# Performance work log

Measured on AMD Instinct MI355X. Metric: run time of the kernel, lower is better.

The kernel has to match this reference:

```python
import jax, jax.numpy as jnp
import numpy as np
import math

L, B, T, S, D, H = 6, 4, 1024, 1024, 1024, 16
HD = D // H
SCALE = 1.0 / math.sqrt(HD)
EPS = 1e-5


def _ln(x, w, b):
    m = x.mean(-1, keepdims=True)
    v = ((x - m) ** 2).mean(-1, keepdims=True)
    return (x - m) * jax.lax.rsqrt(v + EPS) * w + b


def _mha(xq, xkv, qw, qb, kw, kb, vw, vb, ow, ob, mask):
    b, t, _ = xq.shape
    s = xkv.shape[1]
    q = (xq @ qw.T + qb).reshape(b, t, H, HD).transpose(0, 2, 1, 3)
    k = (xkv @ kw.T + kb).reshape(b, s, H, HD).transpose(0, 2, 1, 3)
    v = (xkv @ vw.T + vb).reshape(b, s, H, HD).transpose(0, 2, 1, 3)
    scores = jnp.einsum('bhqd,bhkd->bhqk', q, k) * SCALE
    scores = jnp.where(mask == 0, -jnp.inf, scores)
    attn = jax.nn.softmax(scores, axis=-1)  # dropout is identity (eval)
    o = jnp.einsum('bhqk,bhkd->bhqd', attn, v).transpose(0, 2, 1, 3).reshape(b, t, D)
    return o @ ow.T + ob


def _ffn(x, f1w, f1b, f2w, f2b, fnw, fnb):
    h = jax.nn.gelu(x @ f1w.T + f1b, approximate=False)
    y = h @ f2w.T + f2b
    return x + _ln(y, fnw, fnb)


def setup_inputs() -> dict:
    key = jax.random.key(0)
    ks = jax.random.split(key, 16)
    wf = lambda k: jax.random.normal(k, (L, D, D), jnp.float32) * 0.02
    zb = jnp.zeros((L, D), jnp.float32)
    ones = jnp.ones((L, D), jnp.float32)
    inp = {
        'x': jax.random.normal(ks[0], (B, T, D), jnp.float32),
        'enc_outputs': jax.random.normal(ks[1], (B, S, D), jnp.float32),
        'sqw': wf(ks[2]), 'sqb': zb, 'skw': wf(ks[3]), 'skb': zb,
        'svw': wf(ks[4]), 'svb': zb, 'sow': wf(ks[5]), 'sob': zb,
        'cqw': wf(ks[6]), 'cqb': zb, 'ckw': wf(ks[7]), 'ckb': zb,
        'cvw': wf(ks[8]), 'cvb': zb, 'cow': wf(ks[9]), 'cob': zb,
        'f1w': wf(ks[10]), 'f1b': zb, 'f2w': wf(ks[11]), 'f2b': zb,
        'fnw': ones, 'fnb': zb,
        'l1w': ones, 'l1b': zb, 'l2w': ones, 'l2b': zb, 'l3w': ones, 'l3b': zb,
        'src_mask': jnp.ones((1, 1, T, S), jnp.int32),
        'tgt_mask': jnp.tril(jnp.ones((T, T), jnp.int32))[None, None],
    }
    return inp


def reference(x, enc_outputs, sqw, sqb, skw, skb, svw, svb, sow, sob,
              cqw, cqb, ckw, ckb, cvw, cvb, cow, cob,
              f1w, f1b, f2w, f2b, fnw, fnb,
              l1w, l1b, l2w, l2b, l3w, l3b, src_mask, tgt_mask):
    for l in range(L):
        sa = _mha(x, x, sqw[l], sqb[l], skw[l], skb[l], svw[l], svb[l], sow[l], sob[l], tgt_mask)
        x = _ln(x + sa, l1w[l], l1b[l])
        ca = _mha(x, enc_outputs, cqw[l], cqb[l], ckw[l], ckb[l], cvw[l], cvb[l], cow[l], cob[l], src_mask)
        x = _ln(x + ca, l2w[l], l2b[l])
        ff = _ffn(x, f1w[l], f1b[l], f2w[l], f2b[l], fnw[l], fnb[l])
        x = _ln(x + ff, l3w[l], l3b[l])
    return x
```

## Files before the change

kernel.cpp:

```cpp
#include <hip/hip_runtime.h>
#include <stdint.h>

typedef unsigned short u16;
typedef unsigned int u32;
typedef __bf16 bf16x8 __attribute__((ext_vector_type(8)));
typedef float f32x4 __attribute__((ext_vector_type(4)));
typedef u16 u16x8 __attribute__((ext_vector_type(8)));
typedef u16 u16x4 __attribute__((ext_vector_type(4)));
typedef u32 u32x2 __attribute__((ext_vector_type(2)));

#define MFMA16(A, B, C) __builtin_amdgcn_mfma_f32_16x16x32_bf16((A), (B), (C), 0, 0, 0)

#define GLOAD_LDS16(GP, LP)                                                    \
  __builtin_amdgcn_global_load_lds(                                            \
      (__attribute__((address_space(1))) void*)(GP),                           \
      (__attribute__((address_space(3))) void*)(LP), 16, 0, 0)

__device__ __forceinline__ u16 f2bf(float f) {
  return __builtin_bit_cast(u16, (__bf16)f);
}

__device__ __forceinline__ float bf2f(u16 v) {
  return __builtin_bit_cast(float, ((u32)v) << 16);
}

__device__ __forceinline__ float exp2_raw(float x) {
  float r;
  asm("v_exp_f32 %0, %1\n\ts_nop 0" : "=v"(r) : "v"(x));
  return r;
}

__device__ __forceinline__ u32 cvt_pk_bf16(float lo, float hi) {
  u32 r;
  asm("v_cvt_pk_bf16_f32 %0, %1, %2" : "=v"(r) : "v"(lo), "v"(hi));
  return r;
}

#define SC2 0.1803368801111204f

struct WPtrs {
  const float* p[10];
};

__global__ __launch_bounds__(256) void wcvt_kernel(WPtrs w, u16* __restrict__ dst, int loff,
                                                   int nIter, int perMatUnits) {
  const int mat = blockIdx.y;
  const float4* __restrict__ src = (const float4*)(w.p[mat] + loff);
  u16x8* __restrict__ d = (u16x8*)dst + (size_t)mat * perMatUnits;
  size_t t = (size_t)blockIdx.x * 256 + threadIdx.x;
  for (int it = 0; it < nIter; ++it, t += 65536) {
    float4 v0 = src[t * 2];
    float4 v1 = src[t * 2 + 1];
    u16x8 o = {f2bf(v0.x), f2bf(v0.y), f2bf(v0.z), f2bf(v0.w),
               f2bf(v1.x), f2bf(v1.y), f2bf(v1.z), f2bf(v1.w)};
    d[t] = o;
  }
}

struct GemmArgs {
  const u16* A[3];
  const u16* W[3];
  const float* bias[3];
  u16* C[3];
  float scale[3];
};

__global__ __launch_bounds__(256, 4) void gemm_bt(GemmArgs g) {
  const int mat = blockIdx.y >> 3;
  const int n0 = (blockIdx.y & 7) * 128;
  const int m0 = blockIdx.x * 128;
  const int kz = blockIdx.z;
  const int kn = 16 / gridDim.z;
  const u16* __restrict__ A = g.A[mat];
  const u16* __restrict__ W = g.W[mat];

  __shared__ u16 As[128][64];
  __shared__ u16 Bs[128][64];

  const int tid = threadIdx.x;
  const int lane = tid & 63;
  const int wv = tid >> 6;
  const int wm = (wv >> 1) * 64;
  const int wn = (wv & 1) * 64;
  const int fr = lane & 15;
  const int fg = lane >> 4;

  f32x4 acc[4][4];
#pragma unroll
  for (int i = 0; i < 4; ++i)
#pragma unroll
    for (int j = 0; j < 4; ++j)
#pragma unroll
      for (int r = 0; r < 4; ++r) acc[i][j][r] = 0.f;

  const int row8 = lane >> 3;
  const int csw = ((lane & 7) ^ row8) * 8;
  const u16* ga = A + (size_t)(m0 + wv * 32 + row8) * 1024 + csw + kz * kn * 64;
  const u16* gb = W + (size_t)(n0 + wv * 32 + row8) * 1024 + csw + kz * kn * 64;

  for (int kt = 0; kt < kn; ++kt) {
    __syncthreads();
#pragma unroll
    for (int i = 0; i < 4; ++i) {
      GLOAD_LDS16(ga + (size_t)i * 8 * 1024, &As[wv * 32 + i * 8][0]);
      GLOAD_LDS16(gb + (size_t)i * 8 * 1024, &Bs[wv * 32 + i * 8][0]);
    }
    ga += 64;
    gb += 64;
    __syncthreads();
#pragma unroll
    for (int ks = 0; ks < 2; ++ks) {
      bf16x8 af[4], bfr[4];
#pragma unroll
      for (int i = 0; i < 4; ++i) {
        af[i] = *(const bf16x8*)&As[wm + i * 16 + fr][((ks * 4 + fg) ^ (fr & 7)) * 8];
        bfr[i] = *(const bf16x8*)&Bs[wn + i * 16 + fr][((ks * 4 + fg) ^ (fr & 7)) * 8];
      }
#pragma unroll
      for (int mi = 0; mi < 4; ++mi)
#pragma unroll
        for (int ni = 0; ni < 4; ++ni) acc[mi][ni] = MFMA16(af[mi], bfr[ni], acc[mi][ni]);
    }
  }

  const float* __restrict__ bias = g.bias[mat];
  const float scl = g.scale[mat];
  float bv[4];
#pragma unroll
  for (int ni = 0; ni < 4; ++ni) bv[ni] = (kz == 0) ? bias[n0 + wn + ni * 16 + fr] : 0.f;

  u16* __restrict__ C = g.C[mat] + (size_t)kz * (4096 * 1024);
#pragma unroll
  for (int mi = 0; mi < 4; ++mi) {
#pragma unroll
    for (int ni = 0; ni < 4; ++ni) {
      const int col = n0 + wn + ni * 16 + fr;
#pragma unroll
      for (int r = 0; r < 4; ++r) {
        const int row = m0 + wm + mi * 16 + fg * 4 + r;
        C[(size_t)row * 1024 + col] = f2bf((acc[mi][ni][r] + bv[ni]) * scl);
      }
    }
  }
}

__global__ __launch_bounds__(512, 4) void attn_fwd(const u16* __restrict__ Q,
                                                   const u16* __restrict__ K,
                                                   const u16* __restrict__ V,
                                                   u16* __restrict__ O, int causal) {
  const int b = blockIdx.x >> 4;
  const int h = blockIdx.x & 15;
  const int qb = causal ? (7 - blockIdx.y) : blockIdx.y;
  const int tid = threadIdx.x;
  const int lane = tid & 63;
  const int wv = tid >> 6;
  const int fr = lane & 15;
  const int fg = lane >> 4;

  __shared__ u16 Ks[2][64][64];
  __shared__ u16 Vt[2][64][64];
  __shared__ u16 Plds[8][16][64];

  const int qrow0 = b * 1024 + qb * 128 + wv * 16;
  const int col0 = h * 64;

  const u16* qp = Q + (size_t)(qrow0 + fr) * 1024 + col0 + fg * 8;
  bf16x8 aQ0 = *(const bf16x8*)qp;
  bf16x8 aQ1 = *(const bf16x8*)(qp + 32);

  f32x4 ov[4];
#pragma unroll
  for (int i = 0; i < 4; ++i)
#pragma unroll
    for (int r = 0; r < 4; ++r) ov[i][r] = 0.f;
  float l_part = 0.f;

  const int kv_base = b * 1024;
  const int qg = qb * 128 + wv * 16 + fr;
  const int qg_max = qb * 128 + wv * 16 + 15;
  const int nt = causal ? (2 * qb + 2) : 16;

  const u16* gk0 = K + (size_t)(kv_base + wv * 16 + (lane >> 3)) * 1024 + col0 +
                   (((lane & 7) ^ (lane >> 3)) * 8);
  const int vt = tid - 256;
  const int kkp = vt & 31;
  const int d0 = (vt >> 5) * 8;
  const u16* gv0 = V + (size_t)(kv_base + 2 * kkp) * 1024 + col0 + d0;

#define STAGE_K(T, BUF)                                                        \
  if (wv < 4) {                                                                \
    const u16* gk = gk0 + (size_t)(T)*64 * 1024;                               \
    GLOAD_LDS16(gk, &Ks[BUF][wv * 16][0]);                                     \
    GLOAD_LDS16(gk + 8 * 1024, &Ks[BUF][wv * 16 + 8][0]);                      \
  }
#define LOAD_V(T)                                                              \
  if (tid >= 256) {                                                            \
    const u16* gvp = gv0 + (size_t)(T)*64 * 1024;                              \
    vr0 = *(const u16x8*)gvp;                                                  \
    vr1 = *(const u16x8*)(gvp + 1024);                                         \
  }
#define WRITE_V(BUF)                                                           \
  if (tid >= 256) {                                                            \
    _Pragma("unroll") for (int j = 0; j < 8; ++j) {                            \
      u32 pk = (u32)vr0[j] | ((u32)vr1[j] << 16);                              \
      *(u32*)&Vt[BUF][d0 + j][(((kkp >> 2) ^ j) * 8) + (kkp & 3) * 2] = pk;    \
    }                                                                          \
  }

  u16x8 vr0, vr1;
  STAGE_K(0, 0);
  LOAD_V(0);
  WRITE_V(0);

  for (int t = 0; t < nt; ++t) {
    const int cur = t & 1;
    __syncthreads();
    const bool pf = (t + 1 < nt);
    if (pf) {
      STAGE_K(t + 1, cur ^ 1);
      LOAD_V(t + 1);
    }

    const bool active = !causal || (t * 64 <= qg_max);
    if (active) {
      f32x4 st[4];
      __builtin_amdgcn_s_setprio(1);
#pragma unroll
      for (int hh = 0; hh < 4; ++hh) {
#pragma unroll
        for (int r = 0; r < 4; ++r) st[hh][r] = 0.f;
        const u16* krow = &Ks[cur][hh * 16 + fr][0];
        bf16x8 k0 = *(const bf16x8*)(krow + ((fg ^ (fr & 7)) * 8));
        bf16x8 k1 = *(const bf16x8*)(krow + (((4 + fg) ^ (fr & 7)) * 8));
        st[hh] = MFMA16(k0, aQ0, st[hh]);
        st[hh] = MFMA16(k1, aQ1, st[hh]);
      }
      __builtin_amdgcn_s_setprio(0);

      if (causal && t >= 2 * qb) {
#pragma unroll
        for (int hh = 0; hh < 4; ++hh)
#pragma unroll
          for (int r = 0; r < 4; ++r) {
            const int kkg = t * 64 + hh * 16 + fg * 4 + r;
            if (kkg > qg) st[hh][r] = -1e30f;
          }
      }

      float p[16];
#pragma unroll
      for (int hh = 0; hh < 4; ++hh)
#pragma unroll
        for (int r = 0; r < 4; ++r) {
          const float e = exp2_raw(st[hh][r]);
          p[hh * 4 + r] = e;
          l_part += e;
        }

#pragma unroll
      for (int hh = 0; hh < 4; ++hh) {
        u32x2 wpair = {cvt_pk_bf16(p[hh * 4 + 0], p[hh * 4 + 1]),
                       cvt_pk_bf16(p[hh * 4 + 2], p[hh * 4 + 3])};
        const int c = hh * 2 + (fg >> 1);
        *(u32x2*)&Plds[wv][fr][((c ^ (fr & 7)) * 8) + (fg & 1) * 4] = wpair;
      }
      bf16x8 pa[2];
#pragma unroll
      for (int ks = 0; ks < 2; ++ks)
        pa[ks] = *(const bf16x8*)&Plds[wv][fr][(((ks * 4 + fg) ^ (fr & 7)) * 8)];
      __builtin_amdgcn_s_setprio(1);
#pragma unroll
      for (int dt = 0; dt < 4; ++dt) {
#pragma unroll
        for (int ks = 0; ks < 2; ++ks) {
          bf16x8 bvv =
              *(const bf16x8*)&Vt[cur][dt * 16 + fr][(((ks * 4 + fg) ^ (fr & 7)) * 8)];
          ov[dt] = MFMA16(pa[ks], bvv, ov[dt]);
        }
      }
      __builtin_amdgcn_s_setprio(0);
    }

    if (pf) WRITE_V(cur ^ 1);
  }

  float ps = l_part;
  ps += __shfl_xor(ps, 16);
  ps += __shfl_xor(ps, 32);
  const float linv = 1.0f / ps;
  float fin[4];
#pragma unroll
  for (int r = 0; r < 4; ++r) fin[r] = __shfl(linv, fg * 4 + r);
#pragma unroll
  for (int dt = 0; dt < 4; ++dt)
#pragma unroll
    for (int r = 0; r < 4; ++r) {
      const int row = qrow0 + fg * 4 + r;
      const int col = col0 + dt * 16 + fr;
      O[(size_t)row * 1024 + col] = f2bf(ov[dt][r] * fin[r]);
    }
#undef STAGE_K
#undef LOAD_V
#undef WRITE_V
}

__device__ __forceinline__ float4 ld_bf4(const u16* p, size_t idx4) {
  u16x4 t = ((const u16x4*)p)[idx4];
  return make_float4(bf2f(t[0]), bf2f(t[1]), bf2f(t[2]), bf2f(t[3]));
}

__global__ __launch_bounds__(256) void ln_res_kernel(const u16* __restrict__ Xb_in,
                                                     const u16* __restrict__ T0,
                                                     const u16* __restrict__ T1, int nT,
                                                     const float* __restrict__ w,
                                                     const float* __restrict__ bia,
                                                     u16* __restrict__ Xb_out) {
  __shared__ float red[2][4];
  const int row = blockIdx.x;
  const int tid = threadIdx.x;
  const int lane = tid & 63, wv = tid >> 6;
  const size_t base4 = (size_t)row * 256;
  float4 xv = ld_bf4(Xb_in, base4 + tid);
  float4 tv = ld_bf4(T0, base4 + tid);
  float z0 = xv.x + tv.x, z1 = xv.y + tv.y, z2 = xv.z + tv.z, z3 = xv.w + tv.w;
  if (nT == 2) {
    float4 t1 = ld_bf4(T1, base4 + tid);
    z0 += t1.x; z1 += t1.y; z2 += t1.z; z3 += t1.w;
  }
  float s = z0 + z1 + z2 + z3;
  float ss = z0 * z0 + z1 * z1 + z2 * z2 + z3 * z3;
#pragma unroll
  for (int m = 1; m <= 32; m <<= 1) {
    s += __shfl_xor(s, m);
    ss += __shfl_xor(ss, m);
  }
  if (lane == 0) {
    red[0][wv] = s;
    red[1][wv] = ss;
  }
  __syncthreads();
  s = red[0][0] + red[0][1] + red[0][2] + red[0][3];
  ss = red[1][0] + red[1][1] + red[1][2] + red[1][3];
  const float mean = s * (1.f / 1024.f);
  const float var = ss * (1.f / 1024.f) - mean * mean;
  const float rs = rsqrtf(fmaxf(var, 0.f) + 1e-5f);
  float4 wv4 = ((const float4*)w)[tid];
  float4 bv4 = ((const float4*)bia)[tid];
  float o0 = (z0 - mean) * rs * wv4.x + bv4.x;
  float o1 = (z1 - mean) * rs * wv4.y + bv4.y;
  float o2 = (z2 - mean) * rs * wv4.z + bv4.z;
  float o3 = (z3 - mean) * rs * wv4.w + bv4.w;
  u16x4 ob = {f2bf(o0), f2bf(o1), f2bf(o2), f2bf(o3)};
  ((u16x4*)Xb_out)[base4 + tid] = ob;
}

__global__ __launch_bounds__(256) void ffn_ln_kernel(
    const u16* __restrict__ Xb, const u16* __restrict__ Y0, const u16* __restrict__ Y1,
    int nT, const float* __restrict__ fw_, const float* __restrict__ fb_,
    const float* __restrict__ w3, const float* __restrict__ b3, u16* __restrict__ Xb_out,
    float* __restrict__ Fout) {
  __shared__ float red[2][4];
  const int row = blockIdx.x;
  const int tid = threadIdx.x;
  const int lane = tid & 63, wv = tid >> 6;
  const size_t base4 = (size_t)row * 256;
  float4 yv = ld_bf4(Y0, base4 + tid);
  if (nT == 2) {
    float4 y1 = ld_bf4(Y1, base4 + tid);
    yv.x += y1.x; yv.y += y1.y; yv.z += y1.z; yv.w += y1.w;
  }
  float s = yv.x + yv.y + yv.z + yv.w;
  float ss = yv.x * yv.x + yv.y * yv.y + yv.z * yv.z + yv.w * yv.w;
#pragma unroll
  for (int m = 1; m <= 32; m <<= 1) {
    s += __shfl_xor(s, m);
    ss += __shfl_xor(ss, m);
  }
  if (lane == 0) {
    red[0][wv] = s;
    red[1][wv] = ss;
  }
  __syncthreads();
  s = red[0][0] + red[0][1] + red[0][2] + red[0][3];
  ss = red[1][0] + red[1][1] + red[1][2] + red[1][3];
  const float mean = s * (1.f / 1024.f);
  const float var = ss * (1.f / 1024.f) - mean * mean;
  const float rs = rsqrtf(fmaxf(var, 0.f) + 1e-5f);
  float4 xv = ld_bf4(Xb, base4 + tid);
  float4 fw4 = ((const float4*)fw_)[tid];
  float4 fb4 = ((const float4*)fb_)[tid];
  float z0 = 2.f * xv.x + (yv.x - mean) * rs * fw4.x + fb4.x;
  float z1 = 2.f * xv.y + (yv.y - mean) * rs * fw4.y + fb4.y;
  float z2 = 2.f * xv.z + (yv.z - mean) * rs * fw4.z + fb4.z;
  float z3 = 2.f * xv.w + (yv.w - mean) * rs * fw4.w + fb4.w;
  float s2 = z0 + z1 + z2 + z3;
  float ss2 = z0 * z0 + z1 * z1 + z2 * z2 + z3 * z3;
#pragma unroll
  for (int m = 1; m <= 32; m <<= 1) {
    s2 += __shfl_xor(s2, m);
    ss2 += __shfl_xor(ss2, m);
  }
  __syncthreads();
  if (lane == 0) {
    red[0][wv] = s2;
    red[1][wv] = ss2;
  }
  __syncthreads();
  s2 = red[0][0] + red[0][1] + red[0][2] + red[0][3];
  ss2 = red[1][0] + red[1][1] + red[1][2] + red[1][3];
  const float mean2 = s2 * (1.f / 1024.f);
  const float var2 = ss2 * (1.f / 1024.f) - mean2 * mean2;
  const float rs2 = rsqrtf(fmaxf(var2, 0.f) + 1e-5f);
  float4 w4 = ((const float4*)w3)[tid];
  float4 b4 = ((const float4*)b3)[tid];
  float o0 = (z0 - mean2) * rs2 * w4.x + b4.x;
  float o1 = (z1 - mean2) * rs2 * w4.y + b4.y;
  float o2 = (z2 - mean2) * rs2 * w4.z + b4.z;
  float o3 = (z3 - mean2) * rs2 * w4.w + b4.w;
  u16x4 ob = {f2bf(o0), f2bf(o1), f2bf(o2), f2bf(o3)};
  ((u16x4*)Xb_out)[base4 + tid] = ob;
  if (Fout) ((float4*)Fout)[base4 + tid] = make_float4(o0, o1, o2, o3);
}

__global__ __launch_bounds__(256) void gelu_combine(const u16* __restrict__ T0,
                                                    const u16* __restrict__ T1, int nT,
                                                    u16* __restrict__ dst) {
  const size_t i = (size_t)blockIdx.x * 256 + threadIdx.x;
  float4 v = ld_bf4(T0, i);
  if (nT == 2) {
    float4 u = ld_bf4(T1, i);
    v.x += u.x; v.y += u.y; v.z += u.z; v.w += u.w;
  }
  v.x = 0.5f * v.x * (1.0f + erff(v.x * 0.70710678118654752f));
  v.y = 0.5f * v.y * (1.0f + erff(v.y * 0.70710678118654752f));
  v.z = 0.5f * v.z * (1.0f + erff(v.z * 0.70710678118654752f));
  v.w = 0.5f * v.w * (1.0f + erff(v.w * 0.70710678118654752f));
  u16x4 o = {f2bf(v.x), f2bf(v.y), f2bf(v.z), f2bf(v.w)};
  ((u16x4*)dst)[i] = o;
}

__global__ __launch_bounds__(256) void cast2_kernel(const float* __restrict__ inA,
                                                    const float* __restrict__ inB,
                                                    u16* __restrict__ outA,
                                                    u16* __restrict__ outB) {
  const int bx = blockIdx.x;
  const float* in = (bx < 4096) ? inA : inB;
  u16* out = (bx < 4096) ? outA : outB;
  const size_t i = (size_t)(bx & 4095) * 256 + threadIdx.x;
  float4 v = ((const float4*)in)[i];
  u16x4 o = {f2bf(v.x), f2bf(v.y), f2bf(v.z), f2bf(v.w)};
  ((u16x4*)out)[i] = o;
}

extern "C" void kernel_launch(void* const* d_in, const int* in_sizes, int n_in, void* d_out,
                              int out_size, void* d_ws, size_t ws_size, hipStream_t stream) {
  const float* x_in = (const float*)d_in[0];
  const float* enc = (const float*)d_in[1];
  const float* sqw = (const float*)d_in[2];
  const float* sqb = (const float*)d_in[3];
  const float* skw = (const float*)d_in[4];
  const float* skb = (const float*)d_in[5];
  const float* svw = (const float*)d_in[6];
  const float* svb = (const float*)d_in[7];
  const float* sow = (const float*)d_in[8];
  const float* sob = (const float*)d_in[9];
  const float* cqw = (const float*)d_in[10];
  const float* cqb = (const float*)d_in[11];
  const float* ckw = (const float*)d_in[12];
  const float* ckb = (const float*)d_in[13];
  const float* cvw = (const float*)d_in[14];
  const float* cvb = (const float*)d_in[15];
  const float* cow = (const float*)d_in[16];
  const float* cob = (const float*)d_in[17];
  const float* f1w = (const float*)d_in[18];
  const float* f1b = (const float*)d_in[19];
  const float* f2w = (const float*)d_in[20];
  const float* f2b = (const float*)d_in[21];
  const float* fnw = (const float*)d_in[22];
  const float* fnb = (const float*)d_in[23];
  const float* l1w = (const float*)d_in[24];
  const float* l1b = (const float*)d_in[25];
  const float* l2w = (const float*)d_in[26];
  const float* l2b = (const float*)d_in[27];
  const float* l3w = (const float*)d_in[28];
  const float* l3b = (const float*)d_in[29];

  const size_t MB = 1024 * 1024;
  const int ALLW = (ws_size >= 200 * MB) ? 1 : 0;
  const int NS = (ws_size >= 90 * MB) ? 2 : 1;
  char* ws = (char*)d_ws;
  u16* tmpb = (u16*)ws;
  char* p = ws + (size_t)NS * 8 * MB;
  u16* xb = (u16*)p;   p += 8 * MB;
  u16* encb = (u16*)p; p += 8 * MB;
  u16* qbuf = (u16*)p; p += 8 * MB;
  u16* kbuf = (u16*)p; p += 8 * MB;
  u16* vbuf = (u16*)p; p += 8 * MB;
  u16* wbf = (u16*)p;
  u16* tmpb1 = tmpb + (size_t)4 * 1024 * 1024;
  const size_t W1M = 1024 * 1024;

  cast2_kernel<<<8192, 256, 0, stream>>>(x_in, enc, xb, encb);

  WPtrs wp;
  wp.p[0] = sqw; wp.p[1] = skw; wp.p[2] = svw; wp.p[3] = sow;
  wp.p[4] = cqw; wp.p[5] = ckw; wp.p[6] = cvw; wp.p[7] = cow;
  wp.p[8] = f1w; wp.p[9] = f2w;

  if (ALLW) wcvt_kernel<<<dim3(256, 10), 256, 0, stream>>>(wp, wbf, 0, 12, 786432);

  for (int l = 0; l < 6; ++l) {
    const size_t bo = (size_t)l * 1024;
    if (!ALLW) wcvt_kernel<<<dim3(256, 10), 256, 0, stream>>>(wp, wbf, l * (int)W1M, 2, 131072);
    #define WT(t) (ALLW ? (wbf + ((size_t)(t)*6 + l) * W1M) : (wbf + (size_t)(t)*W1M))

    GemmArgs g;
    g.scale[0] = SC2; g.scale[1] = 1.f; g.scale[2] = 1.f;
    g.A[0] = xb; g.A[1] = xb; g.A[2] = xb;
    g.W[0] = WT(0); g.W[1] = WT(1); g.W[2] = WT(2);
    g.bias[0] = sqb + bo; g.bias[1] = skb + bo; g.bias[2] = svb + bo;
    g.C[0] = qbuf; g.C[1] = kbuf; g.C[2] = vbuf;
    gemm_bt<<<dim3(32, 24, 1), 256, 0, stream>>>(g);
    attn_fwd<<<dim3(64, 8), 512, 0, stream>>>(qbuf, kbuf, vbuf, qbuf, 1);
    g.scale[0] = 1.f;
    g.A[0] = qbuf; g.W[0] = WT(3); g.bias[0] = sob + bo; g.C[0] = tmpb;
    gemm_bt<<<dim3(32, 8, NS), 256, 0, stream>>>(g);
    ln_res_kernel<<<4096, 256, 0, stream>>>(xb, tmpb, tmpb1, NS, l1w + bo, l1b + bo, xb);

    g.scale[0] = SC2;
    g.A[0] = xb; g.A[1] = encb; g.A[2] = encb;
    g.W[0] = WT(4); g.W[1] = WT(5); g.W[2] = WT(6);
    g.bias[0] = cqb + bo; g.bias[1] = ckb + bo; g.bias[2] = cvb + bo;
    g.C[0] = qbuf; g.C[1] = kbuf; g.C[2] = vbuf;
    gemm_bt<<<dim3(32, 24, 1), 256, 0, stream>>>(g);
    attn_fwd<<<dim3(64, 8), 512, 0, stream>>>(qbuf, kbuf, vbuf, qbuf, 0);
    g.scale[0] = 1.f;
    g.A[0] = qbuf; g.W[0] = WT(7); g.bias[0] = cob + bo; g.C[0] = tmpb;
    gemm_bt<<<dim3(32, 8, NS), 256, 0, stream>>>(g);
    ln_res_kernel<<<4096, 256, 0, stream>>>(xb, tmpb, tmpb1, NS, l2w + bo, l2b + bo, xb);

    g.A[0] = xb; g.W[0] = WT(8); g.bias[0] = f1b + bo; g.C[0] = tmpb;
    gemm_bt<<<dim3(32, 8, NS), 256, 0, stream>>>(g);
    gelu_combine<<<4096, 256, 0, stream>>>(tmpb, tmpb1, NS, kbuf);
    g.A[0] = kbuf; g.W[0] = WT(9); g.bias[0] = f2b + bo; g.C[0] = tmpb;
    gemm_bt<<<dim3(32, 8, NS), 256, 0, stream>>>(g);
    float* fo = (l == 5) ? (float*)d_out : nullptr;
    ffn_ln_kernel<<<4096, 256, 0, stream>>>(xb, tmpb, tmpb1, NS, fnw + bo, fnb + bo, l3w + bo,
                                            l3b + bo, xb, fo);
    #undef WT
  }
}
```

Measured before the change: 1.365 ms.

## Precompute cross-attention K/V for all layers in one batched GEMM upfront

Cross-attention K and V projections depend only on encoder outputs, so all six layers' K/V are computed in a single large GEMM launch before the layer loop and stored in extra workspace. Each layer then only runs the Q projection for cross-attention. The weight conversion kernel is also simplified to one float4 per thread with a larger grid. The total work is unchanged, but the big upfront launch fills the GPU better and leaves less work on the serial per-layer path. In exchange it needs about 96 MB more workspace and falls back to the old path when the workspace is too small.

```diff
diff --git a/kernel.cpp b/kernel.cpp
--- a/kernel.cpp
+++ b/kernel.cpp
@@ -42,19 +42,12 @@
   const float* p[10];
 };
 
-__global__ __launch_bounds__(256) void wcvt_kernel(WPtrs w, u16* __restrict__ dst, int loff,
-                                                   int nIter, int perMatUnits) {
+__global__ __launch_bounds__(256) void wcvt_kernel(WPtrs w, u16* __restrict__ dst, int loff) {
   const int mat = blockIdx.y;
-  const float4* __restrict__ src = (const float4*)(w.p[mat] + loff);
-  u16x8* __restrict__ d = (u16x8*)dst + (size_t)mat * perMatUnits;
-  size_t t = (size_t)blockIdx.x * 256 + threadIdx.x;
-  for (int it = 0; it < nIter; ++it, t += 65536) {
-    float4 v0 = src[t * 2];
-    float4 v1 = src[t * 2 + 1];
-    u16x8 o = {f2bf(v0.x), f2bf(v0.y), f2bf(v0.z), f2bf(v0.w),
-               f2bf(v1.x), f2bf(v1.y), f2bf(v1.z), f2bf(v1.w)};
-    d[t] = o;
-  }
+  const int i = blockIdx.x * 256 + threadIdx.x;
+  float4 v = ((const float4*)(w.p[mat] + loff))[i];
+  u16x4 o = {f2bf(v.x), f2bf(v.y), f2bf(v.z), f2bf(v.w)};
+  ((u16x4*)dst)[(size_t)mat * gridDim.x * 256 + i] = o;
 }
 
 struct GemmArgs {
@@ -139,6 +132,86 @@
       for (int r = 0; r < 4; ++r) {
         const int row = m0 + wm + mi * 16 + fg * 4 + r;
         C[(size_t)row * 1024 + col] = f2bf((acc[mi][ni][r] + bv[ni]) * scl);
+      }
+    }
+  }
+}
+
+__global__ __launch_bounds__(256, 4) void gemm_ckv(const u16* __restrict__ A,
+                                                   const u16* __restrict__ wbf,
+                                                   const float* __restrict__ ckb,
+                                                   const float* __restrict__ cvb,
+                                                   u16* __restrict__ ckv) {
+  const int m = blockIdx.y >> 3;
+  const int l = m >> 1;
+  const int ty = m & 1;
+  const int n0 = (blockIdx.y & 7) * 128;
+  const int m0 = blockIdx.x * 128;
+  const u16* __restrict__ W = wbf + ((size_t)(5 + ty) * 6 + l) * (1024 * 1024);
+  const float* __restrict__ bias = (ty ? cvb : ckb) + l * 1024;
+  u16* __restrict__ C = ckv + (size_t)m * (4096 * 1024);
+
+  __shared__ u16 As[128][64];
+  __shared__ u16 Bs[128][64];
+
+  const int tid = threadIdx.x;
+  const int lane = tid & 63;
+  const int wv = tid >> 6;
+  const int wm = (wv >> 1) * 64;
+  const int wn = (wv & 1) * 64;
+  const int fr = lane & 15;
+  const int fg = lane >> 4;
+
+  f32x4 acc[4][4];
+#pragma unroll
+  for (int i = 0; i < 4; ++i)
+#pragma unroll
+    for (int j = 0; j < 4; ++j)
+#pragma unroll
+      for (int r = 0; r < 4; ++r) acc[i][j][r] = 0.f;
+
+  const int row8 = lane >> 3;
+  const int csw = ((lane & 7) ^ row8) * 8;
+  const u16* ga = A + (size_t)(m0 + wv * 32 + row8) * 1024 + csw;
+  const u16* gb = W + (size_t)(n0 + wv * 32 + row8) * 1024 + csw;
+
+  for (int kt = 0; kt < 16; ++kt) {
+    __syncthreads();
+#pragma unroll
+    for (int i = 0; i < 4; ++i) {
+      GLOAD_LDS16(ga + (size_t)i * 8 * 1024, &As[wv * 32 + i * 8][0]);
+      GLOAD_LDS16(gb + (size_t)i * 8 * 1024, &Bs[wv * 32 + i * 8][0]);
+    }
+    ga += 64;
+    gb += 64;
+    __syncthreads();
+#pragma unroll
+    for (int ks = 0; ks < 2; ++ks) {
+      bf16x8 af[4], bfr[4];
+#pragma unroll
+      for (int i = 0; i < 4; ++i) {
+        af[i] = *(const bf16x8*)&As[wm + i * 16 + fr][((ks * 4 + fg) ^ (fr & 7)) * 8];
+        bfr[i] = *(const bf16x8*)&Bs[wn + i * 16 + fr][((ks * 4 + fg) ^ (fr & 7)) * 8];
+      }
+#pragma unroll
+      for (int mi = 0; mi < 4; ++mi)
+#pragma unroll
+        for (int ni = 0; ni < 4; ++ni) acc[mi][ni] = MFMA16(af[mi], bfr[ni], acc[mi][ni]);
+    }
+  }
+
+  float bv[4];
+#pragma unroll
+  for (int ni = 0; ni < 4; ++ni) bv[ni] = bias[n0 + wn + ni * 16 + fr];
+#pragma unroll
+  for (int mi = 0; mi < 4; ++mi) {
+#pragma unroll
+    for (int ni = 0; ni < 4; ++ni) {
+      const int col = n0 + wn + ni * 16 + fr;
+#pragma unroll
+      for (int r = 0; r < 4; ++r) {
+        const int row = m0 + wm + mi * 16 + fg * 4 + r;
+        C[(size_t)row * 1024 + col] = f2bf(acc[mi][ni][r] + bv[ni]);
       }
     }
   }
@@ -488,6 +561,7 @@
   const size_t MB = 1024 * 1024;
   const int ALLW = (ws_size >= 200 * MB) ? 1 : 0;
   const int NS = (ws_size >= 90 * MB) ? 2 : 1;
+  const int CKV = (ALLW && ws_size >= 273 * MB) ? 1 : 0;
   char* ws = (char*)d_ws;
   u16* tmpb = (u16*)ws;
   char* p = ws + (size_t)NS * 8 * MB;
@@ -496,7 +570,8 @@
   u16* qbuf = (u16*)p; p += 8 * MB;
   u16* kbuf = (u16*)p; p += 8 * MB;
   u16* vbuf = (u16*)p; p += 8 * MB;
-  u16* wbf = (u16*)p;
+  u16* wbf = (u16*)p;  p += (ALLW ? 120 : 20) * MB;
+  u16* ckv = (u16*)p;
   u16* tmpb1 = tmpb + (size_t)4 * 1024 * 1024;
   const size_t W1M = 1024 * 1024;
 
@@ -507,11 +582,12 @@
   wp.p[4] = cqw; wp.p[5] = ckw; wp.p[6] = cvw; wp.p[7] = cow;
   wp.p[8] = f1w; wp.p[9] = f2w;
 
-  if (ALLW) wcvt_kernel<<<dim3(256, 10), 256, 0, stream>>>(wp, wbf, 0, 12, 786432);
+  if (ALLW) wcvt_kernel<<<dim3(6144, 10), 256, 0, stream>>>(wp, wbf, 0);
+  if (CKV) gemm_ckv<<<dim3(32, 96), 256, 0, stream>>>(encb, wbf, ckb, cvb, ckv);
 
   for (int l = 0; l < 6; ++l) {
     const size_t bo = (size_t)l * 1024;
-    if (!ALLW) wcvt_kernel<<<dim3(256, 10), 256, 0, stream>>>(wp, wbf, l * (int)W1M, 2, 131072);
+    if (!ALLW) wcvt_kernel<<<dim3(1024, 10), 256, 0, stream>>>(wp, wbf, l * (int)W1M);
     #define WT(t) (ALLW ? (wbf + ((size_t)(t)*6 + l) * W1M) : (wbf + (size_t)(t)*W1M))
 
     GemmArgs g;
@@ -528,12 +604,25 @@
     ln_res_kernel<<<4096, 256, 0, stream>>>(xb, tmpb, tmpb1, NS, l1w + bo, l1b + bo, xb);
 
     g.scale[0] = SC2;
-    g.A[0] = xb; g.A[1] = encb; g.A[2] = encb;
-    g.W[0] = WT(4); g.W[1] = WT(5); g.W[2] = WT(6);
-    g.bias[0] = cqb + bo; g.bias[1] = ckb + bo; g.bias[2] = cvb + bo;
-    g.C[0] = qbuf; g.C[1] = kbuf; g.C[2] = vbuf;
-    gemm_bt<<<dim3(32, 24, 1), 256, 0, stream>>>(g);
-    attn_fwd<<<dim3(64, 8), 512, 0, stream>>>(qbuf, kbuf, vbuf, qbuf, 0);
+    const u16 *ck_l, *cv_l;
+    if (CKV) {
+      g.A[0] = xb;
+      g.W[0] = WT(4);
+      g.bias[0] = cqb + bo;
+      g.C[0] = qbuf;
+      gemm_bt<<<dim3(32, 8, 1), 256, 0, stream>>>(g);
+      ck_l = ckv + (size_t)(2 * l) * (4096 * 1024);
+      cv_l = ckv + (size_t)(2 * l + 1) * (4096 * 1024);
+    } else {
+      g.A[0] = xb; g.A[1] = encb; g.A[2] = encb;
+      g.W[0] = WT(4); g.W[1] = WT(5); g.W[2] = WT(6);
+      g.bias[0] = cqb + bo; g.bias[1] = ckb + bo; g.bias[2] = cvb + bo;
+      g.C[0] = qbuf; g.C[1] = kbuf; g.C[2] = vbuf;
+      gemm_bt<<<dim3(32, 24, 1), 256, 0, stream>>>(g);
+      ck_l = kbuf;
+      cv_l = vbuf;
+    }
+    attn_fwd<<<dim3(64, 8), 512, 0, stream>>>(qbuf, ck_l, cv_l, qbuf, 0);
     g.scale[0] = 1.f;
     g.A[0] = qbuf; g.W[0] = WT(7); g.bias[0] = cob + bo; g.C[0] = tmpb;
     gemm_bt<<<dim3(32, 8, NS), 256, 0, stream>>>(g);
```

New measurement: 1.478 ms. +8.2%, slower.
